# Optimization experiments

Hardware: AMD Instinct MI355X
Metric: run time of the kernel (lower is better)

Reference implementation:

```python
import jax, jax.numpy as jnp
import numpy as np

SEQ, LABEL, PRED = 96, 48, 96
DEC_LEN = LABEL + PRED  # 144
D_MODEL, N_HEADS, D_FF, C, NF = 512, 8, 2048, 7, 4
E = D_MODEL // N_HEADS  # 64
M_ENC = min(64, SEQ // 2)      # 48 modes, encoder self-attn
M_DEC = min(64, DEC_LEN // 2)  # 64 modes, decoder self / cross-q
M_KV = min(64, SEQ // 2)       # 48 modes, cross-kv
KMA = 25                       # moving-average kernel
E_LAYERS = 2
B = 128


def series_decomp(x):
    # moving average with edge replication padding (matches torch AvgPool1d version)
    p = (KMA - 1) // 2
    xp = jnp.concatenate([jnp.repeat(x[:, :1], p, axis=1), x, jnp.repeat(x[:, -1:], p, axis=1)], axis=1)
    cs = jnp.cumsum(xp, axis=1)
    cs = jnp.concatenate([jnp.zeros_like(cs[:, :1]), cs], axis=1)
    mean = (cs[:, KMA:] - cs[:, :-KMA]) / KMA  # [B,L,C]
    return x - mean, mean


def circ_conv(x, w):
    # Conv1d kernel=3, padding=1, padding_mode='circular', no bias. x [B,L,Cin], w [Cout,Cin,3]
    xp = jnp.concatenate([x[:, -1:], x, x[:, :1]], axis=1)
    return (jnp.einsum('blc,oc->blo', xp[:, :-2], w[:, :, 0])
            + jnp.einsum('blc,oc->blo', xp[:, 1:-1], w[:, :, 1])
            + jnp.einsum('blc,oc->blo', xp[:, 2:], w[:, :, 2]))


def my_layernorm(x, w, b):
    mu = jnp.mean(x, axis=-1, keepdims=True)
    var = jnp.mean((x - mu) ** 2, axis=-1, keepdims=True)
    xh = (x - mu) / jnp.sqrt(var + 1e-5) * w + b
    return xh - jnp.mean(xh, axis=1, keepdims=True)  # subtract per-batch time mean


def embed(x, mark, conv_w, time_w):
    # DataEmbedding_wo_pos: circular token conv + timeF linear (both bias-free)
    return circ_conv(x, conv_w) + mark @ time_w.T


def cplx(w):
    return jax.lax.complex(w[..., 0], w[..., 1])


def fourier_block(q, w, L):
    # q [B,L,H,E]; w complex [H,E,E,M]; low-frequency mode select -> first M rfft bins
    x = jnp.transpose(q, (0, 2, 3, 1))      # [B,H,E,L]
    x_ft = jnp.fft.rfft(x, axis=-1)
    M = w.shape[-1]
    out_sel = jnp.einsum('bhem,heom->bhom', x_ft[..., :M], w)
    out_ft = jnp.zeros_like(x_ft).at[..., :M].set(out_sel)
    return jnp.fft.irfft(out_ft, n=L, axis=-1)  # [B,H,E,L]


def fourier_cross(q, k, w, Lq):
    # FourierCrossAttention, activation='tanh' (complex tanh); v unused as in original
    xq_ft = jnp.fft.rfft(jnp.transpose(q, (0, 2, 3, 1)), axis=-1)[..., :M_DEC]
    xk_ft = jnp.fft.rfft(jnp.transpose(k, (0, 2, 3, 1)), axis=-1)[..., :M_KV]
    xqk = jnp.tanh(jnp.einsum('bhex,bhey->bhxy', xq_ft, xk_ft))
    xqkv = jnp.einsum('bhxy,bhey->bhex', xqk, xk_ft)
    xqkvw = jnp.einsum('bhex,heox->bhox', xqkv, w)
    out_ft = jnp.zeros(xqkvw.shape[:-1] + (Lq // 2 + 1,), dtype=xqkvw.dtype)
    out_ft = out_ft.at[..., :M_DEC].set(xqkvw)
    return jnp.fft.irfft(out_ft / (D_MODEL * D_MODEL), n=Lq, axis=-1)  # [B,H,E,Lq]


def attn_layer(inner, q_in, k_in, v_in, qw, qb, kw, kb, vw, vb, ow, ob):
    Bb, L, _ = q_in.shape
    S = k_in.shape[1]
    q = (q_in @ qw.T + qb).reshape(Bb, L, N_HEADS, E)
    k = (k_in @ kw.T + kb).reshape(Bb, S, N_HEADS, E)
    v = (v_in @ vw.T + vb).reshape(Bb, S, N_HEADS, E)
    out = inner(q, k, v)                   # [B,H,E,L]
    out = out.reshape(Bb, L, N_HEADS * E)  # row-major reinterpret, matches torch .view quirk
    return out @ ow.T + ob


def _forward(x_enc, x_mark_enc, x_dec, x_mark_dec,
             enc_emb_conv_w, enc_emb_time_w, dec_emb_conv_w, dec_emb_time_w,
             enc_qw, enc_qb, enc_kw, enc_kb, enc_vw, enc_vb, enc_ow, enc_ob,
             enc_fw, enc_c1, enc_c2, enc_norm_w, enc_norm_b,
             ds_qw, ds_qb, ds_kw, ds_kb, ds_vw, ds_vb, ds_ow, ds_ob, ds_fw,
             dc_qw, dc_qb, dc_kw, dc_kb, dc_vw, dc_vb, dc_ow, dc_ob, dc_fw,
             dec_c1, dec_c2, dec_trend_w, dec_norm_w, dec_norm_b, proj_w, proj_b):
    Bb = x_enc.shape[0]
    mean = jnp.broadcast_to(jnp.mean(x_enc, axis=1, keepdims=True), (Bb, PRED, C))
    seasonal_init, trend_init = series_decomp(x_enc)
    seasonal_init = jnp.pad(seasonal_init[:, -LABEL:, :], ((0, 0), (0, PRED), (0, 0)))
    trend_init = jnp.concatenate([trend_init[:, -LABEL:, :], mean], axis=1)

    # encoder
    x = embed(x_enc, x_mark_enc, enc_emb_conv_w, enc_emb_time_w)
    for l in range(E_LAYERS):
        fw = cplx(enc_fw[l])
        new_x = attn_layer(lambda q, k, v: fourier_block(q, fw, SEQ),
                           x, x, x, enc_qw[l], enc_qb[l], enc_kw[l], enc_kb[l],
                           enc_vw[l], enc_vb[l], enc_ow[l], enc_ob[l])
        x, _ = series_decomp(x + new_x)
        y = jax.nn.gelu(jnp.einsum('bld,fd->blf', x, enc_c1[l]), approximate=False)
        y = jnp.einsum('blf,df->bld', y, enc_c2[l])
        x, _ = series_decomp(x + y)
    enc_out = my_layernorm(x, enc_norm_w, enc_norm_b)

    # decoder (single layer)
    x = embed(seasonal_init, x_mark_dec, dec_emb_conv_w, dec_emb_time_w)
    fw_s = cplx(ds_fw)
    fw_c = cplx(dc_fw)
    x = x + attn_layer(lambda q, k, v: fourier_block(q, fw_s, DEC_LEN),
                       x, x, x, ds_qw, ds_qb, ds_kw, ds_kb, ds_vw, ds_vb, ds_ow, ds_ob)
    x, t1 = series_decomp(x)
    x = x + attn_layer(lambda q, k, v: fourier_cross(q, k, fw_c, DEC_LEN),
                       x, enc_out, enc_out, dc_qw, dc_qb, dc_kw, dc_kb, dc_vw, dc_vb, dc_ow, dc_ob)
    x, t2 = series_decomp(x)
    y = jax.nn.gelu(jnp.einsum('bld,fd->blf', x, dec_c1), approximate=False)
    y = jnp.einsum('blf,df->bld', y, dec_c2)
    x, t3 = series_decomp(x + y)
    residual_trend = circ_conv(t1 + t2 + t3, dec_trend_w)  # [B,144,C]
    trend = trend_init + residual_trend
    x = my_layernorm(x, dec_norm_w, dec_norm_b)
    seasonal = x @ proj_w.T + proj_b
    return (trend + seasonal)[:, -PRED:, :]


def setup_inputs() -> dict:
    keys = iter(jax.random.split(jax.random.key(0), 64))

    def n(shape, s=0.02):
        return jax.random.normal(next(keys), shape, dtype=jnp.float32) * s

    def u(shape):
        # torch.rand cfloat scaled by 1/(in_ch*out_ch), stored as trailing (re,im) pair
        return jax.random.uniform(next(keys), shape, dtype=jnp.float32) / (D_MODEL * D_MODEL)

    return dict(
        x_enc=jax.random.normal(next(keys), (B, SEQ, C), dtype=jnp.float32),
        x_mark_enc=jax.random.normal(next(keys), (B, SEQ, NF), dtype=jnp.float32),
        x_dec=jax.random.normal(next(keys), (B, DEC_LEN, C), dtype=jnp.float32),
        x_mark_dec=jax.random.normal(next(keys), (B, DEC_LEN, NF), dtype=jnp.float32),
        enc_emb_conv_w=n((D_MODEL, C, 3)),
        enc_emb_time_w=n((D_MODEL, NF)),
        dec_emb_conv_w=n((D_MODEL, C, 3)),
        dec_emb_time_w=n((D_MODEL, NF)),
        enc_qw=n((E_LAYERS, D_MODEL, D_MODEL)), enc_qb=n((E_LAYERS, D_MODEL)),
        enc_kw=n((E_LAYERS, D_MODEL, D_MODEL)), enc_kb=n((E_LAYERS, D_MODEL)),
        enc_vw=n((E_LAYERS, D_MODEL, D_MODEL)), enc_vb=n((E_LAYERS, D_MODEL)),
        enc_ow=n((E_LAYERS, D_MODEL, D_MODEL)), enc_ob=n((E_LAYERS, D_MODEL)),
        enc_fw=u((E_LAYERS, N_HEADS, E, E, M_ENC, 2)),
        enc_c1=n((E_LAYERS, D_FF, D_MODEL)), enc_c2=n((E_LAYERS, D_MODEL, D_FF)),
        enc_norm_w=jnp.ones((D_MODEL,), jnp.float32), enc_norm_b=jnp.zeros((D_MODEL,), jnp.float32),
        ds_qw=n((D_MODEL, D_MODEL)), ds_qb=n((D_MODEL,)),
        ds_kw=n((D_MODEL, D_MODEL)), ds_kb=n((D_MODEL,)),
        ds_vw=n((D_MODEL, D_MODEL)), ds_vb=n((D_MODEL,)),
        ds_ow=n((D_MODEL, D_MODEL)), ds_ob=n((D_MODEL,)),
        ds_fw=u((N_HEADS, E, E, M_DEC, 2)),
        dc_qw=n((D_MODEL, D_MODEL)), dc_qb=n((D_MODEL,)),
        dc_kw=n((D_MODEL, D_MODEL)), dc_kb=n((D_MODEL,)),
        dc_vw=n((D_MODEL, D_MODEL)), dc_vb=n((D_MODEL,)),
        dc_ow=n((D_MODEL, D_MODEL)), dc_ob=n((D_MODEL,)),
        dc_fw=u((N_HEADS, E, E, M_DEC, 2)),
        dec_c1=n((D_FF, D_MODEL)), dec_c2=n((D_MODEL, D_FF)),
        dec_trend_w=n((C, D_MODEL, 3)),
        dec_norm_w=jnp.ones((D_MODEL,), jnp.float32), dec_norm_b=jnp.zeros((D_MODEL,), jnp.float32),
        proj_w=n((C, D_MODEL)), proj_b=jnp.zeros((C,), jnp.float32),
    )


def reference(x_enc, x_mark_enc, x_dec, x_mark_dec,
              enc_emb_conv_w, enc_emb_time_w, dec_emb_conv_w, dec_emb_time_w,
              enc_qw, enc_qb, enc_kw, enc_kb, enc_vw, enc_vb, enc_ow, enc_ob,
              enc_fw, enc_c1, enc_c2, enc_norm_w, enc_norm_b,
              ds_qw, ds_qb, ds_kw, ds_kb, ds_vw, ds_vb, ds_ow, ds_ob, ds_fw,
              dc_qw, dc_qb, dc_kw, dc_kb, dc_vw, dc_vb, dc_ow, dc_ob, dc_fw,
              dec_c1, dec_c2, dec_trend_w, dec_norm_w, dec_norm_b, proj_w, proj_b):
    return _forward(x_enc, x_mark_enc, x_dec, x_mark_dec,
                    enc_emb_conv_w, enc_emb_time_w, dec_emb_conv_w, dec_emb_time_w,
                    enc_qw, enc_qb, enc_kw, enc_kb, enc_vw, enc_vb, enc_ow, enc_ob,
                    enc_fw, enc_c1, enc_c2, enc_norm_w, enc_norm_b,
                    ds_qw, ds_qb, ds_kw, ds_kb, ds_vw, ds_vb, ds_ow, ds_ob, ds_fw,
                    dc_qw, dc_qb, dc_kw, dc_kb, dc_vw, dc_vb, dc_ow, dc_ob, dc_fw,
                    dec_c1, dec_c2, dec_trend_w, dec_norm_w, dec_norm_b, proj_w, proj_b)
```

## Files before the change

### kernel.cpp

```cpp
#include <hip/hip_runtime.h>
#include <hip/hip_bf16.h>
#include <math.h>


#define PI_F 3.14159265358979323846f

typedef short bf16x8 __attribute__((ext_vector_type(8)));
typedef float f32x4 __attribute__((ext_vector_type(4)));

static __device__ __forceinline__ int iclamp(int v, int lo, int hi) {
    return v < lo ? lo : (v > hi ? hi : v);
}
static __device__ __forceinline__ unsigned pack2(float x, float y) {
    unsigned xu = __float_as_uint(x) + 0x8000u;
    unsigned yu = __float_as_uint(y) + 0x8000u;
    return (xu >> 16) | (yu & 0xFFFF0000u);
}
static __device__ __forceinline__ unsigned short bfr(float x) {
    return (unsigned short)((__float_as_uint(x) + 0x8000u) >> 16);
}
static __device__ __forceinline__ float bf2f(unsigned short s) {
    return __uint_as_float((unsigned)s << 16);
}

__global__ void zero_out_kernel(float* __restrict__ out, int n) {
    int i = blockIdx.x * 256 + threadIdx.x;
    if (i < n) out[i] = 0.f;
}

struct F2BArgs {
    const float* s[11];
    unsigned short* d[11];
    int boff[12];
};
__global__ void f2b_multi(F2BArgs a) {
    int blk = blockIdx.x;
    int seg = 0;
    while (blk >= a.boff[seg + 1]) seg++;
    int i = (blk - a.boff[seg]) * 1024 + threadIdx.x * 4;
    const float4 v = *(const float4*)(a.s[seg] + i);
    *(uint2*)(a.d[seg] + i) = make_uint2(pack2(v.x, v.y), pack2(v.z, v.w));
}

__global__ void preprocess_kernel(const float* __restrict__ xe,
                                  float* __restrict__ SI, float* __restrict__ TI) {
    int idx = blockIdx.x * 256 + threadIdx.x;
    if (idx >= 128 * 144 * 7) return;
    int c = idx % 7;
    int l = (idx / 7) % 144;
    int b = idx / (7 * 144);
    const float* xb = xe + (size_t)b * 96 * 7;
    if (l < 48) {
        int p = 48 + l;
        float sum = 0.f;
        for (int j = -12; j <= 12; j++) sum += xb[iclamp(p + j, 0, 95) * 7 + c];
        float ma = sum * (1.0f / 25.0f);
        SI[idx] = xb[p * 7 + c] - ma;
        TI[idx] = ma;
    } else {
        SI[idx] = 0.f;
        float m = 0.f;
        for (int l2 = 0; l2 < 96; l2++) m += xb[l2 * 7 + c];
        TI[idx] = m * (1.0f / 96.0f);
    }
}

__global__ void embed_feat(const float* __restrict__ x, const float* __restrict__ mark,
                           unsigned short* __restrict__ F, int L) {
    int row = blockIdx.x * 256 + threadIdx.x;
    if (row >= 128 * L) return;
    int l = row % L;
    int b = row / L;
    int lm = (l == 0) ? L - 1 : l - 1;
    int lp = (l == L - 1) ? 0 : l + 1;
    const float* x0 = x + (size_t)b * L * 7;
    const float* mk = mark + (size_t)row * 4;
    union { unsigned short s[64]; uint4 u[8]; } f;
#pragma unroll
    for (int k = 0; k < 8; k++) f.u[k] = make_uint4(0u, 0u, 0u, 0u);
#pragma unroll
    for (int c = 0; c < 7; c++) {
        f.s[c * 3 + 0] = bfr(x0[lm * 7 + c]);
        f.s[c * 3 + 1] = bfr(x0[l * 7 + c]);
        f.s[c * 3 + 2] = bfr(x0[lp * 7 + c]);
    }
#pragma unroll
    for (int j = 0; j < 4; j++) f.s[21 + j] = bfr(mk[j]);
    uint4* dst = (uint4*)(F + (size_t)row * 64);
#pragma unroll
    for (int k = 0; k < 8; k++) dst[k] = f.u[k];
}

__global__ void embed_wpack(const float* __restrict__ cw, const float* __restrict__ tw,
                            unsigned short* __restrict__ Wc) {
    int o = blockIdx.x * 256 + threadIdx.x;
    if (o >= 512) return;
    union { unsigned short s[64]; uint4 u[8]; } f;
#pragma unroll
    for (int k = 0; k < 8; k++) f.u[k] = make_uint4(0u, 0u, 0u, 0u);
#pragma unroll
    for (int c = 0; c < 7; c++) {
        const float* w = cw + (o * 7 + c) * 3;
        f.s[c * 3 + 0] = bfr(w[0]);
        f.s[c * 3 + 1] = bfr(w[1]);
        f.s[c * 3 + 2] = bfr(w[2]);
    }
#pragma unroll
    for (int j = 0; j < 4; j++) f.s[21 + j] = bfr(tw[o * 4 + j]);
    uint4* dst = (uint4*)(Wc + (size_t)o * 64);
#pragma unroll
    for (int k = 0; k < 8; k++) dst[k] = f.u[k];
}

__global__ __launch_bounds__(256, 4) void gemm_bb(
    const unsigned short* __restrict__ A, const unsigned short* __restrict__ W,
    const float* __restrict__ bias, float* __restrict__ Cf,
    unsigned short* __restrict__ Cb,
    int N, int K, int lda, int ldw, int gelu, int accum) {
    __shared__ unsigned short As[128 * 64];
    __shared__ unsigned short Ws[128 * 64];
    const int tid = threadIdx.x;
    const int lane = tid & 63, wv = tid >> 6;
    const int wm = (wv & 1) * 64, wn = (wv >> 1) * 64;
    const int q = lane >> 4, ln = lane & 15;
    const size_t bm = (size_t)blockIdx.y * 128;
    const size_t bn = (size_t)blockIdx.x * 128;

    f32x4 acc[4][4];
#pragma unroll
    for (int i = 0; i < 4; i++)
#pragma unroll
        for (int j = 0; j < 4; j++) acc[i][j] = (f32x4){0.f, 0.f, 0.f, 0.f};

    for (int k0 = 0; k0 < K; k0 += 64) {
#pragma unroll
        for (int t = 0; t < 4; t++) {
            int idx = (wv * 4 + t) * 64 + lane;
            int row = idx >> 3, cp = idx & 7;
            int cl = cp ^ (row & 7);
            __builtin_amdgcn_global_load_lds(
                (const __attribute__((address_space(1))) void*)(A + (bm + row) * lda + k0 + cl * 8),
                (__attribute__((address_space(3))) void*)(As + (size_t)(wv * 4 + t) * 512),
                16, 0, 0);
            __builtin_amdgcn_global_load_lds(
                (const __attribute__((address_space(1))) void*)(W + (bn + row) * ldw + k0 + cl * 8),
                (__attribute__((address_space(3))) void*)(Ws + (size_t)(wv * 4 + t) * 512),
                16, 0, 0);
        }
        __syncthreads();
#pragma unroll
        for (int kk = 0; kk < 64; kk += 32) {
            bf16x8 af[4], bfr4[4];
            const int cq = (kk >> 3) + q;
#pragma unroll
            for (int i = 0; i < 4; i++) {
                int r = wm + i * 16 + ln;
                af[i] = *(const bf16x8*)(As + r * 64 + ((cq ^ (r & 7)) * 8));
                int rw = wn + i * 16 + ln;
                bfr4[i] = *(const bf16x8*)(Ws + rw * 64 + ((cq ^ (rw & 7)) * 8));
            }
#pragma unroll
            for (int i = 0; i < 4; i++)
#pragma unroll
                for (int j = 0; j < 4; j++)
                    acc[i][j] = __builtin_amdgcn_mfma_f32_16x16x32_bf16(
                        af[i], bfr4[j], acc[i][j], 0, 0, 0);
        }
        __syncthreads();
    }
#pragma unroll
    for (int j = 0; j < 4; j++) {
        int col = (int)bn + wn + j * 16 + ln;
        float bv = bias ? bias[col] : 0.f;
#pragma unroll
        for (int i = 0; i < 4; i++) {
            size_t row0 = bm + wm + i * 16 + q * 4;
#pragma unroll
            for (int r = 0; r < 4; r++) {
                float v = acc[i][j][r] + bv;
                if (gelu) v = 0.5f * v * (1.f + erff(v * 0.70710678118654752f));
                if (Cf) {
                    float* p = Cf + (row0 + r) * N + col;
                    if (accum) v += *p;
                    *p = v;
                }
                if (Cb) Cb[(row0 + r) * N + col] = bfr(v);
            }
        }
    }
}

__global__ void dtab_kernel(unsigned short* __restrict__ T, int M, int L, int ldk) {
    int i = blockIdx.x * 256 + threadIdx.x;
    if (i >= 128 * ldk) return;
    int n = i / ldk, k = i - n * ldk;
    float val = 0.f;
    if (n < 2 * M && k < L) {
        int m = n >> 1;
        int r = (m * k) % L;
        float ang = -2.f * PI_F * (float)r / (float)L;
        val = (n & 1) ? sinf(ang) : cosf(ang);
    }
    T[i] = bfr(val);
}
__global__ void itab_kernel(unsigned short* __restrict__ T, int M, int L, int K) {
    int i = blockIdx.x * 256 + threadIdx.x;
    if (i >= L * K) return;
    int n = i / K, k = i - n * K;
    int m = k >> 1;
    float c = (m == 0) ? 1.f : 2.f;
    int r = (m * n) % L;
    float ang = 2.f * PI_F * (float)r / (float)L;
    float val = (k & 1) ? -c * sinf(ang) : c * cosf(ang);
    T[i] = bfr(val);
}

__global__ __launch_bounds__(256) void dft_mfma2(
    const unsigned short* __restrict__ P, const unsigned short* __restrict__ Tdb,
    unsigned short* __restrict__ XT, int L, int ldk, int M) {
    __shared__ unsigned short tile[128 * 130];
    const int tid = threadIdx.x;
    const int lane = tid & 63, wv = tid >> 6;
    const int wm = (wv & 1) * 64, wn = (wv >> 1) * 64;
    const int q = lane >> 4, ln = lane & 15;
    const int bm = blockIdx.y;
    const int b = bm >> 2, c0 = (bm & 3) * 128;
    const int h0 = c0 >> 6;
    const unsigned short* Pb = P + (size_t)b * L * 512;

    f32x4 acc[4][4];
#pragma unroll
    for (int i = 0; i < 4; i++)
#pragma unroll
        for (int j = 0; j < 4; j++) acc[i][j] = (f32x4){0.f, 0.f, 0.f, 0.f};

    for (int k0 = 0; k0 < L; k0 += 32) {
        bf16x8 af[4], bf[4];
        union FR { bf16x8 v; unsigned short s[8]; };
#pragma unroll
        for (int i = 0; i < 4; i++) {
            int c = c0 + wm + i * 16 + ln;
            FR fr;
#pragma unroll
            for (int t = 0; t < 8; t++) {
                int l = k0 + q * 8 + t;
                fr.s[t] = (l < L) ? Pb[(size_t)l * 512 + c] : (unsigned short)0;
            }
            af[i] = fr.v;
        }
#pragma unroll
        for (int j = 0; j < 4; j++) {
            int n = wn + j * 16 + ln;
            bf[j] = *(const bf16x8*)(Tdb + (size_t)n * ldk + k0 + q * 8);
        }
#pragma unroll
        for (int i = 0; i < 4; i++)
#pragma unroll
            for (int j = 0; j < 4; j++)
                acc[i][j] = __builtin_amdgcn_mfma_f32_16x16x32_bf16(
                    af[i], bf[j], acc[i][j], 0, 0, 0);
    }
#pragma unroll
    for (int j = 0; j < 4; j++) {
        int col = wn + j * 16 + ln;
#pragma unroll
        for (int i = 0; i < 4; i++) {
            int r0 = wm + i * 16 + q * 4;
#pragma unroll
            for (int r = 0; r < 4; r++)
                tile[(r0 + r) * 130 + col] = bfr(acc[i][j][r]);
        }
    }
    __syncthreads();
    unsigned* XTu = (unsigned*)XT;
    for (int idx = tid; idx < 2 * M * 64; idx += 256) {
        int chunk = idx >> 6, e = idx & 63;
        int h2 = chunk / M, m = chunk - h2 * M;
        unsigned v = *(const unsigned*)&tile[(h2 * 64 + e) * 130 + 2 * m];
        XTu[((size_t)((h0 + h2) * M + m) * 128 + b) * 64 + e] = v;
    }
}

__global__ __launch_bounds__(256) void wtrans3(
    const float* __restrict__ w, unsigned short* __restrict__ WB, int M) {
    __shared__ float Lre[16 * 289], Lim[16 * 289];
    const int h = blockIdx.y;
    const int ot = blockIdx.x >> 1, et = blockIdx.x & 1;
    const int o0 = ot * 8, e0 = et * 32;
    const int tid = threadIdx.x;
    unsigned* WBu = (unsigned*)WB;
    for (int mc = 0; mc < M; mc += 16) {
        for (int idx = tid; idx < 4096; idx += 256) {
            int e = idx >> 7, o = (idx >> 4) & 7, mm = idx & 15;
            const float2 v = *(const float2*)(
                w + ((((size_t)h * 64 + e0 + e) * 64 + o0 + o) * M + mc + mm) * 2);
            Lre[mm * 289 + e * 9 + o] = v.x;
            Lim[mm * 289 + e * 9 + o] = v.y;
        }
        __syncthreads();
        for (int widx = tid; widx < 8192; widx += 256) {
            int mm = widx >> 9, no = (widx >> 5) & 15, e = widx & 31;
            int ol = no >> 1, qn = no & 1;
            float re = Lre[mm * 289 + e * 9 + ol];
            float im = Lim[mm * 289 + e * 9 + ol];
            unsigned v = qn ? pack2(im, re) : pack2(re, -im);
            WBu[((size_t)(h * M + mc + mm) * 128 + 2 * (o0 + ol) + qn) * 64 + e0 + e] = v;
        }
        __syncthreads();
    }
}

__global__ __launch_bounds__(256) void mix_v2(
    const unsigned short* __restrict__ XT, const unsigned short* __restrict__ WB,
    unsigned short* __restrict__ Yp, int M) {
    __shared__ unsigned short tile[128 * 130];
    const int m = blockIdx.x, h = blockIdx.y;
    const int tid = threadIdx.x;
    const int lane = tid & 63, wv = tid >> 6;
    const int wm = (wv & 1) * 64, wn = (wv >> 1) * 64;
    const int q = lane >> 4, ln = lane & 15;
    const size_t hm = (size_t)h * M + m;
    const unsigned short* Ab = XT + hm * 16384;
    const unsigned short* Bb = WB + hm * 16384;

    f32x4 acc[4][4];
#pragma unroll
    for (int i = 0; i < 4; i++)
#pragma unroll
        for (int j = 0; j < 4; j++) acc[i][j] = (f32x4){0.f, 0.f, 0.f, 0.f};

#pragma unroll
    for (int k0 = 0; k0 < 128; k0 += 32) {
        bf16x8 af[4], bf[4];
#pragma unroll
        for (int i = 0; i < 4; i++)
            af[i] = *(const bf16x8*)(Ab + (size_t)(wm + i * 16 + ln) * 128 + k0 + q * 8);
#pragma unroll
        for (int j = 0; j < 4; j++)
            bf[j] = *(const bf16x8*)(Bb + (size_t)(wn + j * 16 + ln) * 128 + k0 + q * 8);
#pragma unroll
        for (int i = 0; i < 4; i++)
#pragma unroll
            for (int j = 0; j < 4; j++)
                acc[i][j] = __builtin_amdgcn_mfma_f32_16x16x32_bf16(
                    af[i], bf[j], acc[i][j], 0, 0, 0);
    }
#pragma unroll
    for (int j = 0; j < 4; j++) {
        int col = wn + j * 16 + ln;
#pragma unroll
        for (int i = 0; i < 4; i++) {
            int r0 = wm + i * 16 + q * 4;
#pragma unroll
            for (int r = 0; r < 4; r++)
                tile[(r0 + r) * 130 + col] = bfr(acc[i][j][r]);
        }
    }
    __syncthreads();
    unsigned* Yu = (unsigned*)Yp;
    for (int idx = tid; idx < 128 * 64; idx += 256) {
        int b = idx >> 6, dw = idx & 63;
        unsigned v = *(const unsigned*)&tile[b * 130 + 2 * dw];
        Yu[(hm * 128 + b) * 64 + dw] = v;
    }
}

__global__ __launch_bounds__(256) void idft_v2(
    const unsigned short* __restrict__ Yp, const unsigned short* __restrict__ Tib,
    unsigned short* __restrict__ Out, int L, int K, int M, float s) {
    __shared__ unsigned short sh[2 * 64 * 132];
    const int tid = threadIdx.x;
    const int lane = tid & 63, wv = tid >> 6;
    const int wm = (wv & 1) * 64, wn = (wv >> 1) * 64;
    const int q = lane >> 4, ln = lane & 15;
    const int bm = blockIdx.y;
    const int b = bm >> 2, h0 = (bm & 3) * 2;
    const int bn = blockIdx.x * 128;

    const unsigned* Yu = (const unsigned*)Yp;
    for (int idx = tid; idx < 2 * M * 64; idx += 256) {
        int chunk = idx >> 6, dw = idx & 63;
        int h2 = chunk / M, m = chunk - h2 * M;
        unsigned v = Yu[((size_t)((h0 + h2) * M + m) * 128 + b) * 64 + dw];
        *(unsigned*)&sh[chunk * 132 + 2 * dw] = v;
    }
    __syncthreads();

    f32x4 acc[4][4];
#pragma unroll
    for (int i = 0; i < 4; i++)
#pragma unroll
        for (int j = 0; j < 4; j++) acc[i][j] = (f32x4){0.f, 0.f, 0.f, 0.f};

    for (int k0 = 0; k0 < K; k0 += 32) {
        bf16x8 af[4], bf[4];
        union FR { bf16x8 v; unsigned u[4]; };
#pragma unroll
        for (int i = 0; i < 4; i++) {
            int lr = wm + i * 16 + ln;
            int h2 = lr >> 6, o = lr & 63;
            FR fr;
#pragma unroll
            for (int jj = 0; jj < 4; jj++) {
                int m = (k0 >> 1) + q * 4 + jj;
                fr.u[jj] = *(const unsigned*)&sh[(h2 * M + m) * 132 + 2 * o];
            }
            af[i] = fr.v;
        }
#pragma unroll
        for (int j = 0; j < 4; j++) {
            int n = bn + wn + j * 16 + ln;
            if (n < L) bf[j] = *(const bf16x8*)(Tib + (size_t)n * K + k0 + q * 8);
            else bf[j] = (bf16x8){0, 0, 0, 0, 0, 0, 0, 0};
        }
#pragma unroll
        for (int i = 0; i < 4; i++)
#pragma unroll
            for (int j = 0; j < 4; j++)
                acc[i][j] = __builtin_amdgcn_mfma_f32_16x16x32_bf16(
                    af[i], bf[j], acc[i][j], 0, 0, 0);
    }
#pragma unroll
    for (int j = 0; j < 4; j++) {
        int col = bn + wn + j * 16 + ln;
        if (col >= L) continue;
#pragma unroll
        for (int i = 0; i < 4; i++) {
            int row0 = bm * 128 + wm + i * 16 + q * 4;
#pragma unroll
            for (int r = 0; r < 4; r++)
                Out[(size_t)(row0 + r) * L + col] = bfr(acc[i][j][r] * s);
        }
    }
}

__global__ __launch_bounds__(256) void xqk3(
    const unsigned short* __restrict__ XTQ, const unsigned short* __restrict__ XTK,
    unsigned* __restrict__ G) {
    __shared__ __align__(16) unsigned char sm[43520];
    unsigned short* Qs = (unsigned short*)sm;
    unsigned short* Bs = (unsigned short*)(sm + 17408);
    float* Ss = (float*)sm;
    const int b = blockIdx.x, h = blockIdx.y;
    const int tid = threadIdx.x;
    const int lane = tid & 63, wv = tid >> 6;
    const int wm = (wv & 1) * 32, wn = (wv >> 1) * 48;
    const int q = lane >> 4, ln = lane & 15;

    const uint4* Qg = (const uint4*)XTQ;
    for (int i = tid; i < 64 * 16; i += 256) {
        int x = i >> 4, c = i & 15;
        *(uint4*)(Qs + x * 136 + c * 8) = Qg[((size_t)(h * 64 + x) * 128 + b) * 16 + c];
    }
    const unsigned* Ku = (const unsigned*)XTK;
    unsigned* Bu = (unsigned*)Bs;
    for (int i = tid; i < 48 * 64; i += 256) {
        int y = i >> 6, e = i & 63;
        unsigned v = Ku[((size_t)(h * 48 + y) * 128 + b) * 64 + e];
        Bu[y * 68 + e] = v ^ 0x80000000u;
        Bu[(48 + y) * 68 + e] = (v >> 16) | (v << 16);
    }
    __syncthreads();

    f32x4 acc[2][3];
#pragma unroll
    for (int i = 0; i < 2; i++)
#pragma unroll
        for (int j = 0; j < 3; j++) acc[i][j] = (f32x4){0.f, 0.f, 0.f, 0.f};

#pragma unroll
    for (int k0 = 0; k0 < 128; k0 += 32) {
        bf16x8 af[2], bf[3];
#pragma unroll
        for (int i = 0; i < 2; i++)
            af[i] = *(const bf16x8*)(Qs + (wm + i * 16 + ln) * 136 + k0 + q * 8);
#pragma unroll
        for (int j = 0; j < 3; j++)
            bf[j] = *(const bf16x8*)(Bs + (wn + j * 16 + ln) * 136 + k0 + q * 8);
#pragma unroll
        for (int i = 0; i < 2; i++)
#pragma unroll
            for (int j = 0; j < 3; j++)
                acc[i][j] = __builtin_amdgcn_mfma_f32_16x16x32_bf16(
                    af[i], bf[j], acc[i][j], 0, 0, 0);
    }
    __syncthreads();
#pragma unroll
    for (int j = 0; j < 3; j++) {
        int col = wn + j * 16 + ln;
#pragma unroll
        for (int i = 0; i < 2; i++) {
            int r0 = wm + i * 16 + q * 4;
#pragma unroll
            for (int r = 0; r < 4; r++)
                Ss[(r0 + r) * 100 + col] = acc[i][j][r];
        }
    }
    __syncthreads();
    for (int i = tid; i < 3072; i += 256) {
        int x = i / 48, y = i - x * 48;
        float re = Ss[x * 100 + y], im = Ss[x * 100 + 48 + y];
        float a2 = 2.f * re, b2 = 2.f * im;
        a2 = fminf(fmaxf(a2, -80.f), 80.f);
        float denom = coshf(a2) + cosf(b2);
        G[((size_t)(b * 8 + h) * 64 + x) * 48 + y] =
            pack2(sinhf(a2) / denom, sinf(b2) / denom);
    }
}

__global__ __launch_bounds__(256) void xqkv3(
    const unsigned* __restrict__ G, const unsigned short* __restrict__ XTK,
    unsigned short* __restrict__ VT) {
    __shared__ __align__(16) unsigned char sm[26624];
    unsigned short* Bs = (unsigned short*)sm;
    unsigned short* Vs = (unsigned short*)sm;
    const int b = blockIdx.x, h = blockIdx.y;
    const int tid = threadIdx.x;
    const int lane = tid & 63, wv = tid >> 6;
    const int wm = (wv & 1) * 32, wn = (wv >> 1) * 64;
    const int q = lane >> 4, ln = lane & 15;

    const unsigned* Ku = (const unsigned*)XTK;
    unsigned* Bu = (unsigned*)Bs;
    for (int i = tid; i < 48 * 64; i += 256) {
        int y = i >> 6, e = i & 63;
        unsigned v = Ku[((size_t)(h * 48 + y) * 128 + b) * 64 + e];
        Bu[(2 * e) * 52 + y] = v ^ 0x80000000u;
        Bu[(2 * e + 1) * 52 + y] = (v >> 16) | (v << 16);
    }
    __syncthreads();

    const unsigned short* Ag = (const unsigned short*)G + (size_t)(b * 8 + h) * 6144;
    f32x4 acc[2][4];
#pragma unroll
    for (int i = 0; i < 2; i++)
#pragma unroll
        for (int j = 0; j < 4; j++) acc[i][j] = (f32x4){0.f, 0.f, 0.f, 0.f};

#pragma unroll
    for (int k0 = 0; k0 < 96; k0 += 32) {
        bf16x8 af[2], bf[4];
#pragma unroll
        for (int i = 0; i < 2; i++)
            af[i] = *(const bf16x8*)(Ag + (wm + i * 16 + ln) * 96 + k0 + q * 8);
#pragma unroll
        for (int j = 0; j < 4; j++)
            bf[j] = *(const bf16x8*)(Bs + (wn + j * 16 + ln) * 104 + k0 + q * 8);
#pragma unroll
        for (int i = 0; i < 2; i++)
#pragma unroll
            for (int j = 0; j < 4; j++)
                acc[i][j] = __builtin_amdgcn_mfma_f32_16x16x32_bf16(
                    af[i], bf[j], acc[i][j], 0, 0, 0);
    }
    __syncthreads();
#pragma unroll
    for (int j = 0; j < 4; j++) {
        int col = wn + j * 16 + ln;
#pragma unroll
        for (int i = 0; i < 2; i++) {
            int r0 = wm + i * 16 + q * 4;
#pragma unroll
            for (int r = 0; r < 4; r++)
                Vs[(r0 + r) * 132 + col] = bfr(acc[i][j][r]);
        }
    }
    __syncthreads();
    unsigned* Vu = (unsigned*)VT;
    for (int i = tid; i < 64 * 64; i += 256) {
        int x = i >> 6, dw = i & 63;
        Vu[((size_t)(h * 64 + x) * 128 + b) * 64 + dw] = *(unsigned*)&Vs[x * 132 + 2 * dw];
    }
}

__global__ void decomp_kernel(const float* __restrict__ P, const float* __restrict__ Q,
                              float* __restrict__ SO, unsigned short* __restrict__ SOb,
                              float* __restrict__ TS, int L, int tmode) {
    int b = blockIdx.x, d0 = blockIdx.y * 64;
    __shared__ float s[144 * 64];
    for (int i = threadIdx.x; i < L * 64; i += 256) {
        int l = i >> 6, d = i & 63;
        size_t idx = ((size_t)b * L + l) * 512 + d0 + d;
        float v = P[idx];
        if (Q) v += Q[idx];
        s[i] = v;
    }
    __syncthreads();
    for (int i = threadIdx.x; i < L * 64; i += 256) {
        int l = i >> 6, d = i & 63;
        float sum = 0.f;
#pragma unroll
        for (int j = -12; j <= 12; j++) sum += s[iclamp(l + j, 0, L - 1) * 64 + d];
        float ma = sum * (1.0f / 25.0f);
        size_t idx = ((size_t)b * L + l) * 512 + d0 + d;
        float so = s[i] - ma;
        SO[idx] = so;
        if (SOb) SOb[idx] = bfr(so);
        if (tmode == 1) TS[idx] = ma;
        else if (tmode == 2) TS[idx] += ma;
    }
}

__global__ __launch_bounds__(256) void ln_rows_kernel(const float* __restrict__ in,
                                                      const float* __restrict__ w,
                                                      const float* __restrict__ bvec,
                                                      float* __restrict__ out) {
    size_t row = blockIdx.x;
    const float* p = in + row * 512;
    int t = threadIdx.x;
    float v0 = p[t], v1 = p[t + 256];
    float s = v0 + v1, s2 = v0 * v0 + v1 * v1;
    for (int o = 32; o > 0; o >>= 1) {
        s += __shfl_xor(s, o, 64);
        s2 += __shfl_xor(s2, o, 64);
    }
    __shared__ float rs[4], rs2[4];
    int wid = t >> 6;
    if ((t & 63) == 0) { rs[wid] = s; rs2[wid] = s2; }
    __syncthreads();
    s = rs[0] + rs[1] + rs[2] + rs[3];
    s2 = rs2[0] + rs2[1] + rs2[2] + rs2[3];
    float mu = s * (1.0f / 512.0f);
    float var = s2 * (1.0f / 512.0f) - mu * mu;
    float r = rsqrtf(var + 1e-5f);
    out[row * 512 + t] = (v0 - mu) * r * w[t] + bvec[t];
    out[row * 512 + t + 256] = (v1 - mu) * r * w[t + 256] + bvec[t + 256];
}

__global__ void timesub_kernel(float* __restrict__ X, unsigned short* __restrict__ Xb,
                               int L) {
    int b = blockIdx.x, d0 = blockIdx.y * 64;
    __shared__ float tile[144 * 64];
    __shared__ float mean[64];
    for (int i = threadIdx.x; i < L * 64; i += 256) {
        int l = i >> 6, d = i & 63;
        tile[i] = X[((size_t)b * L + l) * 512 + d0 + d];
    }
    __syncthreads();
    if (threadIdx.x < 64) {
        float sm = 0.f;
        for (int l = 0; l < L; l++) sm += tile[l * 64 + threadIdx.x];
        mean[threadIdx.x] = sm / (float)L;
    }
    __syncthreads();
    for (int i = threadIdx.x; i < L * 64; i += 256) {
        int l = i >> 6, d = i & 63;
        size_t idx = ((size_t)b * L + l) * 512 + d0 + d;
        float v = tile[i] - mean[d];
        X[idx] = v;
        if (Xb) Xb[idx] = bfr(v);
    }
}

__global__ __launch_bounds__(256) void final_v2(
    const float* __restrict__ XL, const float* __restrict__ TS,
    const float* __restrict__ TI, const float* __restrict__ trend_w,
    const float* __restrict__ proj_w, const float* __restrict__ proj_b,
    float* __restrict__ out) {
    int blk = blockIdx.x;
    int b = blk / 96, lo = blk - b * 96;
    int l = lo + 48;
    int lm = l - 1;
    int lp = (l == 143) ? 0 : l + 1;
    const float* ts = TS + (size_t)b * 144 * 512;
    const float* r0 = ts + (size_t)lm * 512;
    const float* r1 = ts + (size_t)l * 512;
    const float* r2 = ts + (size_t)lp * 512;
    const float* xl = XL + ((size_t)b * 144 + l) * 512;
    int t = threadIdx.x;
    float p[7];
#pragma unroll
    for (int c = 0; c < 7; c++) p[c] = 0.f;
#pragma unroll
    for (int dd = 0; dd < 2; dd++) {
        int d = t + dd * 256;
        float a0 = r0[d], a1 = r1[d], a2 = r2[d], x = xl[d];
#pragma unroll
        for (int c = 0; c < 7; c++) {
            const float* tw = trend_w + ((size_t)c * 512 + d) * 3;
            float v = a0 * tw[0] + a1 * tw[1] + a2 * tw[2];
            v = fmaf(x, proj_w[c * 512 + d], v);
            p[c] += v;
        }
    }
#pragma unroll
    for (int o = 32; o > 0; o >>= 1)
#pragma unroll
        for (int c = 0; c < 7; c++) p[c] += __shfl_xor(p[c], o, 64);
    __shared__ float red[4][7];
    int wid = t >> 6;
    if ((t & 63) == 0)
#pragma unroll
        for (int c = 0; c < 7; c++) red[wid][c] = p[c];
    __syncthreads();
    if (t < 7) {
        float v = red[0][t] + red[1][t] + red[2][t] + red[3][t]
                + TI[((size_t)b * 144 + l) * 7 + t] + proj_b[t];
        out[(size_t)blk * 7 + t] = v;
    }
}

static inline int cdiv(int a, int b) { return (a + b - 1) / b; }

extern "C" void kernel_launch(void* const* d_in, const int* in_sizes, int n_in,
                              void* d_out, int out_size, void* d_ws, size_t ws_size,
                              hipStream_t stream) {
    const float* x_enc      = (const float*)d_in[0];
    const float* x_mark_enc = (const float*)d_in[1];
    const float* x_mark_dec = (const float*)d_in[3];
    const float* enc_emb_conv_w = (const float*)d_in[4];
    const float* enc_emb_time_w = (const float*)d_in[5];
    const float* dec_emb_conv_w = (const float*)d_in[6];
    const float* dec_emb_time_w = (const float*)d_in[7];
    const float* enc_qw = (const float*)d_in[8];
    const float* enc_qb = (const float*)d_in[9];
    const float* enc_ow = (const float*)d_in[14];
    const float* enc_ob = (const float*)d_in[15];
    const float* enc_fw = (const float*)d_in[16];
    const float* enc_c1 = (const float*)d_in[17];
    const float* enc_c2 = (const float*)d_in[18];
    const float* enc_norm_w = (const float*)d_in[19];
    const float* enc_norm_b = (const float*)d_in[20];
    const float* ds_qw = (const float*)d_in[21];
    const float* ds_qb = (const float*)d_in[22];
    const float* ds_ow = (const float*)d_in[27];
    const float* ds_ob = (const float*)d_in[28];
    const float* ds_fw = (const float*)d_in[29];
    const float* dc_qw = (const float*)d_in[30];
    const float* dc_qb = (const float*)d_in[31];
    const float* dc_kw = (const float*)d_in[32];
    const float* dc_kb = (const float*)d_in[33];
    const float* dc_ow = (const float*)d_in[36];
    const float* dc_ob = (const float*)d_in[37];
    const float* dc_fw = (const float*)d_in[38];
    const float* dec_c1 = (const float*)d_in[39];
    const float* dec_c2 = (const float*)d_in[40];
    const float* dec_trend_w = (const float*)d_in[41];
    const float* dec_norm_w = (const float*)d_in[42];
    const float* dec_norm_b = (const float*)d_in[43];
    const float* proj_w = (const float*)d_in[44];
    const float* proj_b = (const float*)d_in[45];

    float* ws = (float*)d_ws;
    float* XD   = ws;
    float* TS   = ws + 9437184;
    float* XE   = ws + 18874368;
    unsigned short* XEb = (unsigned short*)(ws + 25165824);
    unsigned short* XDb = (unsigned short*)(ws + 28311552);
    float* SI   = ws + 33030144;
    float* TI   = ws + 33159168;
    float* TAB  = ws + 33288192;
    unsigned short* WF = (unsigned short*)(ws + 33320960);
    float* SC   = ws + 37646336;
    unsigned short* TdbE = (unsigned short*)(TAB);
    unsigned short* TdbD = (unsigned short*)(TAB + 6144);
    unsigned short* TibE = (unsigned short*)(TAB + 16384);
    unsigned short* TibD = (unsigned short*)(TAB + 20992);
    unsigned short* Fb  = (unsigned short*)(ws + 51277824);
    unsigned short* Wcb = (unsigned short*)(ws + 51867648);

    unsigned short* enc_qw_b = WF;
    unsigned short* enc_ow_b = WF + 524288;
    unsigned short* enc_c1_b = WF + 1048576;
    unsigned short* enc_c2_b = WF + 3145728;
    unsigned short* ds_qw_b  = WF + 5242880;
    unsigned short* ds_ow_b  = WF + 5505024;
    unsigned short* dc_qw_b  = WF + 5767168;
    unsigned short* dc_kw_b  = WF + 6029312;
    unsigned short* dc_ow_b  = WF + 6291456;
    unsigned short* dec_c1_b = WF + 6553600;
    unsigned short* dec_c2_b = WF + 7602176;

    const size_t need_bytes = (size_t)53768192 * sizeof(float);
    if (ws_size < need_bytes) {
        zero_out_kernel<<<cdiv(out_size, 256), 256, 0, stream>>>((float*)d_out, out_size);
        return;
    }

    auto gemm = [&](const unsigned short* A, const unsigned short* W, const float* bias,
                    float* Cf, unsigned short* Cb, int rows, int N, int K,
                    int lda, int ldw, int gelu, int accum) {
        dim3 g(N / 128, rows / 128);
        gemm_bb<<<g, 256, 0, stream>>>(A, W, bias, Cf, Cb, N, K, lda, ldw, gelu, accum);
    };

    {
        F2BArgs fa;
        const float* srcs[11] = {enc_qw, enc_ow, enc_c1, enc_c2, ds_qw, ds_ow,
                                 dc_qw, dc_kw, dc_ow, dec_c1, dec_c2};
        unsigned short* dsts[11] = {enc_qw_b, enc_ow_b, enc_c1_b, enc_c2_b, ds_qw_b,
                                    ds_ow_b, dc_qw_b, dc_kw_b, dc_ow_b, dec_c1_b, dec_c2_b};
        const int ns[11] = {524288, 524288, 2097152, 2097152, 262144, 262144,
                            262144, 262144, 262144, 1048576, 1048576};
        int off = 0;
        fa.boff[0] = 0;
        for (int i = 0; i < 11; i++) {
            fa.s[i] = srcs[i];
            fa.d[i] = dsts[i];
            off += ns[i] / 1024;
            fa.boff[i + 1] = off;
        }
        f2b_multi<<<off, 256, 0, stream>>>(fa);
    }

    dtab_kernel<<<cdiv(128 * 96, 256), 256, 0, stream>>>(TdbE, 48, 96, 96);
    dtab_kernel<<<cdiv(128 * 160, 256), 256, 0, stream>>>(TdbD, 64, 144, 160);
    itab_kernel<<<cdiv(96 * 96, 256), 256, 0, stream>>>(TibE, 48, 96, 96);
    itab_kernel<<<cdiv(144 * 128, 256), 256, 0, stream>>>(TibD, 64, 144, 128);

    preprocess_kernel<<<cdiv(128 * 144 * 7, 256), 256, 0, stream>>>(x_enc, SI, TI);
    embed_wpack<<<2, 256, 0, stream>>>(enc_emb_conv_w, enc_emb_time_w, Wcb);
    embed_feat<<<48, 256, 0, stream>>>(x_enc, x_mark_enc, Fb, 96);
    gemm(Fb, Wcb, nullptr, XE, XEb, 12288, 512, 64, 64, 64, 0, 0);

    for (int l = 0; l < 2; l++) {
        const unsigned short* qwb = enc_qw_b + (size_t)l * 262144;
        const float* qb = enc_qb + (size_t)l * 512;
        const unsigned short* owb = enc_ow_b + (size_t)l * 262144;
        const float* ob = enc_ob + (size_t)l * 512;
        const float* fw = enc_fw + (size_t)l * 8 * 64 * 64 * 48 * 2;
        const unsigned short* c1b = enc_c1_b + (size_t)l * 1048576;
        const unsigned short* c2b = enc_c2_b + (size_t)l * 1048576;
        unsigned short* Pq = (unsigned short*)(SC);
        unsigned short* XT = (unsigned short*)(SC + 3145728);
        unsigned short* WB = (unsigned short*)(SC + 6291456);
        unsigned short* Yp = (unsigned short*)(SC + 9437184);
        unsigned short* Tidb = (unsigned short*)(SC);
        float* To = SC + 3145728;

        gemm(XEb, qwb, qb, nullptr, Pq, 12288, 512, 512, 512, 512, 0, 0);
        dft_mfma2<<<dim3(1, 512), 256, 0, stream>>>(Pq, TdbE, XT, 96, 96, 48);
        wtrans3<<<dim3(16, 8), 256, 0, stream>>>(fw, WB, 48);
        mix_v2<<<dim3(48, 8), 256, 0, stream>>>(XT, WB, Yp, 48);
        idft_v2<<<dim3(1, 512), 256, 0, stream>>>(Yp, TibE, Tidb, 96, 96, 48, 1.f / 96.f);
        gemm(Tidb, owb, ob, To, nullptr, 12288, 512, 512, 512, 512, 0, 0);
        decomp_kernel<<<dim3(128, 8), 256, 0, stream>>>(XE, To, XE, XEb, nullptr, 96, 0);
        unsigned short* hid = (unsigned short*)(SC);
        gemm(XEb, c1b, nullptr, nullptr, hid, 12288, 2048, 512, 512, 512, 1, 0);
        gemm(hid, c2b, nullptr, TS, nullptr, 12288, 512, 2048, 2048, 2048, 0, 0);
        decomp_kernel<<<dim3(128, 8), 256, 0, stream>>>(XE, TS, XE, XEb, nullptr, 96, 0);
    }
    ln_rows_kernel<<<12288, 256, 0, stream>>>(XE, enc_norm_w, enc_norm_b, XE);
    timesub_kernel<<<dim3(128, 8), 256, 0, stream>>>(XE, XEb, 96);

    embed_wpack<<<2, 256, 0, stream>>>(dec_emb_conv_w, dec_emb_time_w, Wcb);
    embed_feat<<<72, 256, 0, stream>>>(SI, x_mark_dec, Fb, 144);
    gemm(Fb, Wcb, nullptr, XD, XDb, 18432, 512, 64, 64, 64, 0, 0);

    {
        unsigned short* Pq = (unsigned short*)(SC);
        unsigned short* XT = (unsigned short*)(SC + 4718592);
        unsigned short* WB = (unsigned short*)(SC + 8912896);
        unsigned short* Yp = (unsigned short*)(SC);
        unsigned short* Tidb = (unsigned short*)(SC + 9437184);
        float* To = SC;

        gemm(XDb, ds_qw_b, ds_qb, nullptr, Pq, 18432, 512, 512, 512, 512, 0, 0);
        dft_mfma2<<<dim3(1, 512), 256, 0, stream>>>(Pq, TdbD, XT, 144, 160, 64);
        wtrans3<<<dim3(16, 8), 256, 0, stream>>>(ds_fw, WB, 64);
        mix_v2<<<dim3(64, 8), 256, 0, stream>>>(XT, WB, Yp, 64);
        idft_v2<<<dim3(2, 512), 256, 0, stream>>>(Yp, TibD, Tidb, 144, 128, 64, 1.f / 144.f);
        gemm(Tidb, ds_ow_b, ds_ob, To, nullptr, 18432, 512, 512, 512, 512, 0, 0);
        decomp_kernel<<<dim3(128, 8), 256, 0, stream>>>(XD, To, XD, XDb, TS, 144, 1);
    }

    {
        unsigned short* Pq  = (unsigned short*)(SC);
        unsigned short* XTQ = (unsigned short*)(SC + 4718592);
        unsigned short* Pk  = (unsigned short*)(SC);
        unsigned short* XTK = (unsigned short*)(SC + 8912896);
        unsigned* G         = (unsigned*)(SC);
        unsigned short* VT  = (unsigned short*)(SC + 3145728);
        unsigned short* WB  = (unsigned short*)(SC + 7340032);
        unsigned short* Yp  = (unsigned short*)(SC + 11534336);
        unsigned short* Tidb = (unsigned short*)(SC);
        float* To = SC + 4718592;

        gemm(XDb, dc_qw_b, dc_qb, nullptr, Pq, 18432, 512, 512, 512, 512, 0, 0);
        dft_mfma2<<<dim3(1, 512), 256, 0, stream>>>(Pq, TdbD, XTQ, 144, 160, 64);
        gemm(XEb, dc_kw_b, dc_kb, nullptr, Pk, 12288, 512, 512, 512, 512, 0, 0);
        dft_mfma2<<<dim3(1, 512), 256, 0, stream>>>(Pk, TdbE, XTK, 96, 96, 48);
        xqk3<<<dim3(128, 8), 256, 0, stream>>>(XTQ, XTK, G);
        xqkv3<<<dim3(128, 8), 256, 0, stream>>>(G, XTK, VT);
        wtrans3<<<dim3(16, 8), 256, 0, stream>>>(dc_fw, WB, 64);
        mix_v2<<<dim3(64, 8), 256, 0, stream>>>(VT, WB, Yp, 64);
        idft_v2<<<dim3(2, 512), 256, 0, stream>>>(Yp, TibD, Tidb, 144, 128, 64,
                                                  1.f / (144.f * 262144.f));
        gemm(Tidb, dc_ow_b, dc_ob, To, nullptr, 18432, 512, 512, 512, 512, 0, 0);
        decomp_kernel<<<dim3(128, 8), 256, 0, stream>>>(XD, To, XD, XDb, TS, 144, 2);
    }

    {
        unsigned short* hid = (unsigned short*)(SC);
        float* fout = XE;
        for (int j0 = 0; j0 < 2048; j0 += 1024) {
            gemm(XDb, dec_c1_b + (size_t)j0 * 512, nullptr, nullptr, hid,
                 18432, 1024, 512, 512, 512, 1, 0);
            gemm(hid, dec_c2_b + j0, nullptr, fout, nullptr,
                 18432, 512, 1024, 1024, 2048, 0, j0 > 0);
        }
        decomp_kernel<<<dim3(128, 8), 256, 0, stream>>>(XD, fout, XD, nullptr, TS, 144, 2);
    }

    ln_rows_kernel<<<18432, 256, 0, stream>>>(XD, dec_norm_w, dec_norm_b, XD);
    timesub_kernel<<<dim3(128, 8), 256, 0, stream>>>(XD, nullptr, 144);
    final_v2<<<12288, 256, 0, stream>>>(
        XD, TS, TI, dec_trend_w, proj_w, proj_b, (float*)d_out);
}
```

Measured before the change: 1.512 ms.

## Double-buffer LDS tiles in bf16 GEMM to overlap global loads with MFMA

The GEMM kernel gets two LDS buffers for A and W. Async global-to-LDS loads for the next-but-one k-tile are issued while MFMAs run on the current tile, with vmcnt waits and barriers replacing the old load/sync/compute/sync loop. The goal is to hide global memory latency behind compute. LDS use doubles and launch bounds drop to 2 blocks per CU, which lowers occupancy, and the hand-counted vmcnt(8) is easy to get wrong.

```diff
diff --git a/kernel.cpp b/kernel.cpp
--- a/kernel.cpp
+++ b/kernel.cpp
@@ -112,13 +112,13 @@
     for (int k = 0; k < 8; k++) dst[k] = f.u[k];
 }
 
-__global__ __launch_bounds__(256, 4) void gemm_bb(
+__global__ __launch_bounds__(256, 2) void gemm_bb(
     const unsigned short* __restrict__ A, const unsigned short* __restrict__ W,
     const float* __restrict__ bias, float* __restrict__ Cf,
     unsigned short* __restrict__ Cb,
     int N, int K, int lda, int ldw, int gelu, int accum) {
-    __shared__ unsigned short As[128 * 64];
-    __shared__ unsigned short Ws[128 * 64];
+    __shared__ unsigned short As[2][128 * 64];
+    __shared__ unsigned short Ws[2][128 * 64];
     const int tid = threadIdx.x;
     const int lane = tid & 63, wv = tid >> 6;
     const int wm = (wv & 1) * 64, wn = (wv >> 1) * 64;
@@ -132,7 +132,10 @@
 #pragma unroll
         for (int j = 0; j < 4; j++) acc[i][j] = (f32x4){0.f, 0.f, 0.f, 0.f};
 
-    for (int k0 = 0; k0 < K; k0 += 64) {
+    const int nt = K >> 6;
+
+    auto stage = [&](int kt, int buf) {
+        const int k0 = kt << 6;
 #pragma unroll
         for (int t = 0; t < 4; t++) {
             int idx = (wv * 4 + t) * 64 + lane;
@@ -140,34 +143,49 @@
             int cl = cp ^ (row & 7);
             __builtin_amdgcn_global_load_lds(
                 (const __attribute__((address_space(1))) void*)(A + (bm + row) * lda + k0 + cl * 8),
-                (__attribute__((address_space(3))) void*)(As + (size_t)(wv * 4 + t) * 512),
+                (__attribute__((address_space(3))) void*)(&As[buf][(size_t)(wv * 4 + t) * 512]),
                 16, 0, 0);
             __builtin_amdgcn_global_load_lds(
                 (const __attribute__((address_space(1))) void*)(W + (bn + row) * ldw + k0 + cl * 8),
-                (__attribute__((address_space(3))) void*)(Ws + (size_t)(wv * 4 + t) * 512),
+                (__attribute__((address_space(3))) void*)(&Ws[buf][(size_t)(wv * 4 + t) * 512]),
                 16, 0, 0);
         }
-        __syncthreads();
+    };
+
+    auto compute = [&](int buf) {
 #pragma unroll
         for (int kk = 0; kk < 64; kk += 32) {
-            bf16x8 af[4], bfr4[4];
+            bf16x8 af[4], bw[4];
             const int cq = (kk >> 3) + q;
 #pragma unroll
             for (int i = 0; i < 4; i++) {
                 int r = wm + i * 16 + ln;
-                af[i] = *(const bf16x8*)(As + r * 64 + ((cq ^ (r & 7)) * 8));
+                af[i] = *(const bf16x8*)(&As[buf][r * 64 + ((cq ^ (r & 7)) * 8)]);
                 int rw = wn + i * 16 + ln;
-                bfr4[i] = *(const bf16x8*)(Ws + rw * 64 + ((cq ^ (rw & 7)) * 8));
+                bw[i] = *(const bf16x8*)(&Ws[buf][rw * 64 + ((cq ^ (rw & 7)) * 8)]);
             }
 #pragma unroll
             for (int i = 0; i < 4; i++)
 #pragma unroll
                 for (int j = 0; j < 4; j++)
                     acc[i][j] = __builtin_amdgcn_mfma_f32_16x16x32_bf16(
-                        af[i], bfr4[j], acc[i][j], 0, 0, 0);
-        }
-        __syncthreads();
-    }
+                        af[i], bw[j], acc[i][j], 0, 0, 0);
+        }
+    };
+
+    stage(0, 0);
+    if (nt > 1) stage(1, 1);
+    for (int t = 0; t < nt - 1; t++) {
+        asm volatile("s_waitcnt vmcnt(8)" ::: "memory");
+        __builtin_amdgcn_s_barrier();
+        compute(t & 1);
+        __builtin_amdgcn_s_barrier();
+        if (t + 2 < nt) stage(t + 2, t & 1);
+    }
+    asm volatile("s_waitcnt vmcnt(0)" ::: "memory");
+    __builtin_amdgcn_s_barrier();
+    compute((nt - 1) & 1);
+
 #pragma unroll
     for (int j = 0; j < 4; j++) {
         int col = (int)bn + wn + j * 16 + ln;
```

Result: no change. 1.535 ms (+1.5%).
